# Performance work log

Measured on AMD Instinct MI355X. Metric: run time of the kernel, lower is better.

Reference implementation:

```python
import jax, jax.numpy as jnp
import numpy as np

THETA = 10.0
TOP_K = 12
EPS = 1e-8  # torch F.cosine_similarity eps


def setup_inputs() -> dict:
    key = jax.random.key(0)
    h = jax.random.normal(key, (8192, 512), dtype=jnp.float32)
    return {"h": h}


def reference(h):
    # cosine similarity: normalize with clamped norm like torch (eps=1e-8)
    norm = jnp.linalg.norm(h, axis=-1, keepdims=True)
    hn = h / jnp.maximum(norm, EPS)
    # Sim[i, j] = cos(h[i], h[j]); [N, N]
    Sim = jnp.einsum('id,jd->ij', hn, hn)
    # top-k neighbors per row
    sim_topk, idx_topk = jax.lax.top_k(Sim, TOP_K)          # [N, k]
    beta = jax.nn.softmax(THETA * sim_topk, axis=-1)        # [N, k]
    h_topk = h[idx_topk]                                    # [N, k, d]
    # dropout is identity in eval mode
    h_sim = jnp.einsum('nk,nkd->nd', beta, h_topk)          # [N, d]
    return h_sim
```

## Files before the change

### kernel.cpp

```cpp
#include <hip/hip_runtime.h>
#include <hip/hip_bf16.h>

#define N 8192
#define D 512
#define K_TOP 12
#define THETA 10.0f
#define EPS 1e-8f
#define TAU 0.10f
#define CAPL 6
#define CAPG 192
#define NPAIR 2080
#define NBLK 1024

typedef float f32x16 __attribute__((ext_vector_type(16)));

__device__ __forceinline__ unsigned int bf16_bits_rne(float v) {
    unsigned int u = __float_as_uint(v);
    u += 0x7FFFu + ((u >> 16) & 1u);
    return u >> 16;
}

__device__ __forceinline__ void load16(const unsigned char* g, unsigned char* l) {
    __builtin_amdgcn_global_load_lds(
        (const __attribute__((address_space(1))) unsigned int*)g,
        (__attribute__((address_space(3))) unsigned int*)l, 16, 0, 0);
}

__device__ __forceinline__ void decode_pair(int p, int& it, int& jt) {
    int j = (int)((sqrtf(8.0f * (float)p + 1.0f) - 1.0f) * 0.5f);
    while ((j + 1) * (j + 2) / 2 <= p) ++j;
    while (j * (j + 1) / 2 > p) --j;
    jt = j;
    it = p - j * (j + 1) / 2;
}

__global__ __launch_bounds__(256) void norm_kernel(const float* __restrict__ h,
                                                   unsigned char* __restrict__ hq,
                                                   float* __restrict__ norms,
                                                   int* __restrict__ gcnt,
                                                   int* __restrict__ gflag) {
    int row = blockIdx.x * 4 + (threadIdx.x >> 6);
    int lane = threadIdx.x & 63;
    const float4* hr4 = (const float4*)(h + (size_t)row * D);
    float4 p0 = hr4[lane], p1 = hr4[64 + lane];
    float ss = p0.x * p0.x + p0.y * p0.y + p0.z * p0.z + p0.w * p0.w +
               p1.x * p1.x + p1.y * p1.y + p1.z * p1.z + p1.w * p1.w;
#pragma unroll
    for (int off = 32; off > 0; off >>= 1) ss += __shfl_xor(ss, off, 64);
    float nrm = fmaxf(sqrtf(ss), EPS);
    float inv = 1.0f / nrm;
    if (lane == 0) { gcnt[row] = 0; gflag[row] = 0; norms[row] = nrm; }
    unsigned int w0 = __builtin_amdgcn_cvt_pk_fp8_f32(p0.x * inv, p0.y * inv, 0, false);
    w0 = __builtin_amdgcn_cvt_pk_fp8_f32(p0.z * inv, p0.w * inv, w0, true);
    unsigned int w1 = __builtin_amdgcn_cvt_pk_fp8_f32(p1.x * inv, p1.y * inv, 0, false);
    w1 = __builtin_amdgcn_cvt_pk_fp8_f32(p1.z * inv, p1.w * inv, w1, true);
    unsigned int* q32 = (unsigned int*)(hq + (size_t)row * D);
    q32[lane] = w0;
    q32[64 + lane] = w1;
}

__global__ __launch_bounds__(256, 4) void simfp8_kernel(
        const unsigned char* __restrict__ hq,
        unsigned int* __restrict__ gcand,
        int* __restrict__ gcnt,
        int* __restrict__ gflag) {
    __shared__ unsigned char tiles[2][128 * 128];
    __shared__ int cnt[256];
    __shared__ unsigned int lbuf[256][CAPL];

    const int b = blockIdx.x;
    const int t = threadIdx.x;
    const int wave = t >> 6, lane = t & 63;
    const int wr = (wave >> 1) * 64, wc = (wave & 1) * 64;
    const int lm32 = lane & 31, lg2 = lane >> 5;
    const int rk = lm32 & 7;

    const int srow = t >> 3;
    const int sq = (t & 7) ^ ((t >> 3) & 7);

    cnt[t] = 0;

    auto stage = [&](int ii0, int jj0, int r_) {
        const unsigned char* gA = hq + (size_t)(ii0 + srow) * D + r_ * 128 + sq * 16;
        const unsigned char* gB = hq + (size_t)(jj0 + srow) * D + r_ * 128 + sq * 16;
        unsigned char* lA = &tiles[0][t * 16];
        unsigned char* lB = &tiles[1][t * 16];
#pragma unroll
        for (int e = 0; e < 4; e++) {
            load16(gA + (size_t)(e * 32) * D, lA + e * 4096);
            load16(gB + (size_t)(e * 32) * D, lB + e * 4096);
        }
    };

    const int nloc = (b + 2048 < NPAIR) ? 3 : 2;

    f32x16 acc[2][2];
#pragma unroll
    for (int x = 0; x < 2; x++)
#pragma unroll
        for (int y = 0; y < 2; y++)
#pragma unroll
            for (int q = 0; q < 16; q++) acc[x][y][q] = 0.f;

    for (int qp = 0; qp < nloc; qp++) {
        int it, jt;
        decode_pair(b + qp * NBLK, it, jt);
        const int ci0 = it * 128, cj0 = jt * 128;
        const bool cdiag = (it == jt);

        for (int r = 0; r < 4; r++) {
            __builtin_amdgcn_s_barrier();
            stage(ci0, cj0, r);
            asm volatile("s_waitcnt vmcnt(0)" ::: "memory");
            __builtin_amdgcn_s_barrier();

            __builtin_amdgcn_s_setprio(1);
#pragma unroll
            for (int kk = 0; kk < 8; kk++) {
                const int kb = ((kk ^ rk) << 4) + lg2 * 8;
                long long af[2], bfr[2];
#pragma unroll
                for (int x = 0; x < 2; x++)
                    af[x] = *(const long long*)&tiles[0][(wr + x * 32 + lm32) * 128 + kb];
#pragma unroll
                for (int y = 0; y < 2; y++)
                    bfr[y] = *(const long long*)&tiles[1][(wc + y * 32 + lm32) * 128 + kb];
#pragma unroll
                for (int x = 0; x < 2; x++)
#pragma unroll
                    for (int y = 0; y < 2; y++)
                        acc[x][y] = __builtin_amdgcn_mfma_f32_32x32x16_fp8_fp8(
                            af[x], bfr[y], acc[x][y], 0, 0, 0);
            }
            __builtin_amdgcn_s_setprio(0);
        }

#pragma unroll
        for (int x = 0; x < 2; x++)
#pragma unroll
            for (int y = 0; y < 2; y++) {
                int lcol = wc + y * 32 + lm32;
                int gcol = cj0 + lcol;
#pragma unroll
                for (int q = 0; q < 16; q++) {
                    int rr = wr + x * 32 + (q & 3) + 8 * (q >> 2) + 4 * lg2;
                    int gi = ci0 + rr;
                    float v = acc[x][y][q];
                    acc[x][y][q] = 0.f;
                    if (gi == gcol) v = 1.0f;
                    if (v > TAU) {
                        unsigned int vb = bf16_bits_rne(v) << 16;
                        int idx = atomicAdd(&cnt[rr], 1);
                        if (idx < CAPL) lbuf[rr][idx] = vb | (unsigned int)gcol;
                        else {
                            int pg = atomicAdd(&gcnt[gi], 1);
                            if (pg < CAPG) gcand[(size_t)gi * CAPG + pg] = vb | (unsigned int)gcol;
                            else gflag[gi] = 1;
                        }
                        if (!cdiag) {
                            int idx2 = atomicAdd(&cnt[128 + lcol], 1);
                            if (idx2 < CAPL) lbuf[128 + lcol][idx2] = vb | (unsigned int)gi;
                            else {
                                int pg = atomicAdd(&gcnt[gcol], 1);
                                if (pg < CAPG) gcand[(size_t)gcol * CAPG + pg] = vb | (unsigned int)gi;
                                else gflag[gcol] = 1;
                            }
                        }
                    }
                }
            }

        __syncthreads();
        {
            int grow = (t < 128) ? (ci0 + t) : (cj0 + t - 128);
            int c = cnt[t];
            int s = c < CAPL ? c : CAPL;
            if (s > 0) {
                int base = atomicAdd(&gcnt[grow], s);
                unsigned int* dst = gcand + (size_t)grow * CAPG;
                for (int k = 0; k < s; k++) {
                    int pp = base + k;
                    if (pp < CAPG) dst[pp] = lbuf[t][k];
                    else gflag[grow] = 1;
                }
            }
            cnt[t] = 0;
        }
    }
}

__global__ __launch_bounds__(256) void gather_kernel(const float* __restrict__ h,
                                                     const unsigned char* __restrict__ hq,
                                                     const float* __restrict__ norms,
                                                     const unsigned int* __restrict__ gcand,
                                                     const int* __restrict__ gcnt,
                                                     const int* __restrict__ gflag,
                                                     float* __restrict__ out) {
    int row = blockIdx.x * 4 + (threadIdx.x >> 6);
    int lane = threadIdx.x & 63;

    const float4* hr4 = (const float4*)(h + (size_t)row * D);
    float4 s0 = hr4[lane], s1 = hr4[64 + lane];

    int c = gcnt[row];

    float selv[K_TOP];
    int selj[K_TOP];

    if (c >= K_TOP && c <= CAPG && gflag[row] == 0) {
        const unsigned int* cr = gcand + (size_t)row * CAPG;
        unsigned int e[3];
#pragma unroll
        for (int q = 0; q < 3; q++) {
            int idx = lane + 64 * q;
            e[q] = (idx < c) ? cr[idx] : 0u;
        }
#pragma unroll
        for (int k = 0; k < K_TOP; k++) {
            unsigned int m = e[0];
            if (e[1] > m) m = e[1];
            if (e[2] > m) m = e[2];
#pragma unroll
            for (int off = 32; off > 0; off >>= 1) {
                unsigned int om = __shfl_xor(m, off, 64);
                if (om > m) m = om;
            }
            selv[k] = __uint_as_float(m & 0xFFFF0000u);
            selj[k] = (int)(m & 0x1FFFu);
#pragma unroll
            for (int q = 0; q < 3; q++)
                if (e[q] == m) e[q] = 0u;
        }
    } else {
        float vals[K_TOP];
        int idxs[K_TOP];
#pragma unroll
        for (int q = 0; q < K_TOP; q++) { vals[q] = -3e38f; idxs[q] = 0; }
        float minv = -3e38f;
        int minp = 0;
        const unsigned int* rp = (const unsigned int*)(hq + (size_t)row * D);
        for (int col = lane; col < N; col += 64) {
            const unsigned int* cp = (const unsigned int*)(hq + (size_t)col * D);
            float s = 0.f;
            for (int k4 = 0; k4 < D / 4; k4++) {
                unsigned int ra = rp[k4], ca = cp[k4];
                s += __builtin_amdgcn_cvt_f32_fp8(ra, 0) * __builtin_amdgcn_cvt_f32_fp8(ca, 0);
                s += __builtin_amdgcn_cvt_f32_fp8(ra, 1) * __builtin_amdgcn_cvt_f32_fp8(ca, 1);
                s += __builtin_amdgcn_cvt_f32_fp8(ra, 2) * __builtin_amdgcn_cvt_f32_fp8(ca, 2);
                s += __builtin_amdgcn_cvt_f32_fp8(ra, 3) * __builtin_amdgcn_cvt_f32_fp8(ca, 3);
            }
            if (col == row) s = 1.0f;
            if (s > minv) {
                vals[minp] = s; idxs[minp] = col;
                minv = vals[0]; minp = 0;
#pragma unroll
                for (int q = 1; q < K_TOP; q++)
                    if (vals[q] < minv) { minv = vals[q]; minp = q; }
            }
        }
        for (int k = 0; k < K_TOP; k++) {
            float bv = vals[0]; int bp = 0;
#pragma unroll
            for (int q = 1; q < K_TOP; q++)
                if (vals[q] > bv) { bv = vals[q]; bp = q; }
            float v = bv; int j = idxs[bp]; int src = lane;
#pragma unroll
            for (int off = 32; off > 0; off >>= 1) {
                float ov = __shfl_xor(v, off, 64);
                int oj = __shfl_xor(j, off, 64);
                int os = __shfl_xor(src, off, 64);
                if (ov > v || (ov == v && os < src)) { v = ov; j = oj; src = os; }
            }
            selv[k] = __uint_as_float((unsigned int)(bf16_bits_rne(v) << 16));
            selj[k] = j;
            if (lane == src) vals[bp] = -3e38f;
        }
    }

    unsigned int na[K_TOP], nb[K_TOP];
    float wn[K_TOP];
#pragma unroll
    for (int q = 0; q < K_TOP; q++) {
        const unsigned int* r32 = (const unsigned int*)(hq + (size_t)selj[q] * D);
        na[q] = r32[lane];
        nb[q] = r32[64 + lane];
        wn[q] = norms[selj[q]];
    }

    float mx = selv[0];
    float beta[K_TOP];
    float sum = 0.f;
#pragma unroll
    for (int q = 0; q < K_TOP; q++) { beta[q] = __expf(THETA * (selv[q] - mx)); sum += beta[q]; }
    float rs = 1.0f / sum;

    float acc[8];
#pragma unroll
    for (int ee = 0; ee < 8; ee++) acc[ee] = 0.f;
#pragma unroll
    for (int q = 0; q < K_TOP; q++) {
        float w = beta[q] * rs;
        if (selj[q] == row) {
            acc[0] += w * s0.x; acc[1] += w * s0.y; acc[2] += w * s0.z; acc[3] += w * s0.w;
            acc[4] += w * s1.x; acc[5] += w * s1.y; acc[6] += w * s1.z; acc[7] += w * s1.w;
        } else {
            float wj = w * wn[q];
            acc[0] += wj * __builtin_amdgcn_cvt_f32_fp8(na[q], 0);
            acc[1] += wj * __builtin_amdgcn_cvt_f32_fp8(na[q], 1);
            acc[2] += wj * __builtin_amdgcn_cvt_f32_fp8(na[q], 2);
            acc[3] += wj * __builtin_amdgcn_cvt_f32_fp8(na[q], 3);
            acc[4] += wj * __builtin_amdgcn_cvt_f32_fp8(nb[q], 0);
            acc[5] += wj * __builtin_amdgcn_cvt_f32_fp8(nb[q], 1);
            acc[6] += wj * __builtin_amdgcn_cvt_f32_fp8(nb[q], 2);
            acc[7] += wj * __builtin_amdgcn_cvt_f32_fp8(nb[q], 3);
        }
    }
    float4* o4 = (float4*)(out + (size_t)row * D);
    o4[lane] = make_float4(acc[0], acc[1], acc[2], acc[3]);
    o4[64 + lane] = make_float4(acc[4], acc[5], acc[6], acc[7]);
}

extern "C" void kernel_launch(void* const* d_in, const int* in_sizes, int n_in,
                              void* d_out, int out_size, void* d_ws, size_t ws_size,
                              hipStream_t stream) {
    const float* h = (const float*)d_in[0];
    float* out = (float*)d_out;

    char* ws = (char*)d_ws;
    unsigned char* hq = (unsigned char*)ws;
    size_t off = (size_t)N * D;
    float* norms = (float*)(ws + off);
    int* gcnt = (int*)(ws + off + (size_t)N * 4);
    int* gflag = (int*)(ws + off + (size_t)N * 8);
    unsigned int* gcand = (unsigned int*)(ws + off + (size_t)N * 12);

    norm_kernel<<<N / 4, 256, 0, stream>>>(h, hq, norms, gcnt, gflag);
    simfp8_kernel<<<NBLK, 256, 0, stream>>>(hq, gcand, gcnt, gflag);
    gather_kernel<<<N / 4, 256, 0, stream>>>(h, hq, norms, gcand, gcnt, gflag, out);
}
```

Measured before the change: 135.1 us.

## Pipeline fp8 similarity tiles through a 4-slot LDS ring with prefetch

Splits each 128-byte K stage into 32-byte sub-slices held in a four-slot LDS ring. Loads run two slices ahead, and the prefetch continues across tile-pair boundaries so the next pair's first slices arrive during the current pair's epilogue. Partial vmcnt waits replace the previous load-all-then-compute pattern, aiming to hide global-to-LDS latency behind the MFMAs. The cost is more barriers per tile pair and the removal of the setprio hints, and correctness now depends on careful counter accounting with the epilogue's global atomics and stores in flight.

```diff
diff --git a/kernel.cpp b/kernel.cpp
--- a/kernel.cpp
+++ b/kernel.cpp
@@ -64,7 +64,7 @@
         unsigned int* __restrict__ gcand,
         int* __restrict__ gcnt,
         int* __restrict__ gflag) {
-    __shared__ unsigned char tiles[2][128 * 128];
+    __shared__ unsigned char tiles[4][2][128 * 32];
     __shared__ int cnt[256];
     __shared__ unsigned int lbuf[256][CAPL];
 
@@ -73,26 +73,37 @@
     const int wave = t >> 6, lane = t & 63;
     const int wr = (wave >> 1) * 64, wc = (wave & 1) * 64;
     const int lm32 = lane & 31, lg2 = lane >> 5;
-    const int rk = lm32 & 7;
-
-    const int srow = t >> 3;
-    const int sq = (t & 7) ^ ((t >> 3) & 7);
+    const int rk1 = (lm32 >> 2) & 1;
+
+    const int srow = t >> 1;
+    const int sq = (t & 1) ^ ((t >> 3) & 1);
 
     cnt[t] = 0;
 
-    auto stage = [&](int ii0, int jj0, int r_) {
-        const unsigned char* gA = hq + (size_t)(ii0 + srow) * D + r_ * 128 + sq * 16;
-        const unsigned char* gB = hq + (size_t)(jj0 + srow) * D + r_ * 128 + sq * 16;
-        unsigned char* lA = &tiles[0][t * 16];
-        unsigned char* lB = &tiles[1][t * 16];
-#pragma unroll
-        for (int e = 0; e < 4; e++) {
-            load16(gA + (size_t)(e * 32) * D, lA + e * 4096);
-            load16(gB + (size_t)(e * 32) * D, lB + e * 4096);
-        }
+    auto issue_sub = [&](int ii0, int jj0, int ph) {
+        const unsigned char* gA = hq + (size_t)(ii0 + srow) * D + ph * 32 + sq * 16;
+        const unsigned char* gB = hq + (size_t)(jj0 + srow) * D + ph * 32 + sq * 16;
+        load16(gA, &tiles[ph & 3][0][t * 16]);
+        load16(gB, &tiles[ph & 3][1][t * 16]);
     };
 
     const int nloc = (b + 2048 < NPAIR) ? 3 : 2;
+    const int T = nloc * 16;
+
+    int cit, cjt;
+    decode_pair(b, cit, cjt);
+    int ci0 = cit * 128, cj0 = cjt * 128;
+    bool cdiag = (cit == cjt);
+    int ni0 = 0, nj0 = 0;
+    bool ndiag = false;
+    if (nloc > 1) {
+        int nit, njt;
+        decode_pair(b + NBLK, nit, njt);
+        ni0 = nit * 128; nj0 = njt * 128; ndiag = (nit == njt);
+    }
+
+    issue_sub(ci0, cj0, 0);
+    issue_sub(ci0, cj0, 1);
 
     f32x16 acc[2][2];
 #pragma unroll
@@ -103,28 +114,30 @@
             for (int q = 0; q < 16; q++) acc[x][y][q] = 0.f;
 
     for (int qp = 0; qp < nloc; qp++) {
-        int it, jt;
-        decode_pair(b + qp * NBLK, it, jt);
-        const int ci0 = it * 128, cj0 = jt * 128;
-        const bool cdiag = (it == jt);
-
-        for (int r = 0; r < 4; r++) {
+        for (int g = 0; g < 16; g++) {
+            const int G = qp * 16 + g;
+
+            if (G + 2 < T) {
+                if (g < 14) issue_sub(ci0, cj0, g + 2);
+                else        issue_sub(ni0, nj0, g - 14);
+                asm volatile("s_waitcnt vmcnt(4)" ::: "memory");
+            } else if (G + 1 < T) {
+                asm volatile("s_waitcnt vmcnt(2)" ::: "memory");
+            } else {
+                asm volatile("s_waitcnt vmcnt(0)" ::: "memory");
+            }
             __builtin_amdgcn_s_barrier();
-            stage(ci0, cj0, r);
-            asm volatile("s_waitcnt vmcnt(0)" ::: "memory");
-            __builtin_amdgcn_s_barrier();
-
-            __builtin_amdgcn_s_setprio(1);
-#pragma unroll
-            for (int kk = 0; kk < 8; kk++) {
-                const int kb = ((kk ^ rk) << 4) + lg2 * 8;
+
+#pragma unroll
+            for (int kk = 0; kk < 2; kk++) {
+                const int kb = ((kk ^ rk1) << 4) + lg2 * 8;
                 long long af[2], bfr[2];
 #pragma unroll
                 for (int x = 0; x < 2; x++)
-                    af[x] = *(const long long*)&tiles[0][(wr + x * 32 + lm32) * 128 + kb];
+                    af[x] = *(const long long*)&tiles[g & 3][0][(wr + x * 32 + lm32) * 32 + kb];
 #pragma unroll
                 for (int y = 0; y < 2; y++)
-                    bfr[y] = *(const long long*)&tiles[1][(wc + y * 32 + lm32) * 128 + kb];
+                    bfr[y] = *(const long long*)&tiles[g & 3][1][(wc + y * 32 + lm32) * 32 + kb];
 #pragma unroll
                 for (int x = 0; x < 2; x++)
 #pragma unroll
@@ -132,7 +145,6 @@
                         acc[x][y] = __builtin_amdgcn_mfma_f32_32x32x16_fp8_fp8(
                             af[x], bfr[y], acc[x][y], 0, 0, 0);
             }
-            __builtin_amdgcn_s_setprio(0);
         }
 
 #pragma unroll
@@ -170,7 +182,8 @@
                 }
             }
 
-        __syncthreads();
+        asm volatile("s_waitcnt lgkmcnt(0)" ::: "memory");
+        __builtin_amdgcn_s_barrier();
         {
             int grow = (t < 128) ? (ci0 + t) : (cj0 + t - 128);
             int c = cnt[t];
@@ -185,6 +198,13 @@
                 }
             }
             cnt[t] = 0;
+        }
+
+        ci0 = ni0; cj0 = nj0; cdiag = ndiag;
+        if (qp + 2 < nloc) {
+            int nit, njt;
+            decode_pair(b + (qp + 2) * NBLK, nit, njt);
+            ni0 = nit * 128; nj0 = njt * 128; ndiag = (nit == njt);
         }
     }
 }
```

After: 142.1 us. 1.05x slower.
